# Kernel optimization log

Measured on AMD Instinct MI355X. Metric: run time of the kernel, lower is better.

Reference implementation:

```python
import jax, jax.numpy as jnp
import numpy as np
from jax import lax

B, C, H, T = 128, 64, 32, 256


def _xavier(key, shape):
    fan_out, fan_in = shape[-2], shape[-1]
    s = np.sqrt(6.0 / (fan_in + fan_out)).astype(np.float32)
    return jax.random.uniform(key, shape, jnp.float32, -s, s)


def setup_inputs() -> dict:
    key = jax.random.key(0)
    ks = jax.random.split(key, 12)
    x = jax.random.normal(ks[0], (B, C, T), jnp.float32)
    m = jax.random.uniform(ks[1], (B, C, T), jnp.float32)
    d = jax.random.uniform(ks[2], (B, C, T), jnp.float32)
    Wf = _xavier(ks[3], (C, H, H))
    Vf = _xavier(ks[4], (C, H, 3))
    cf = _xavier(ks[5], (C, H, 1))[:, :, 0]          # (C, H)
    Wb = _xavier(ks[6], (C, H, H))
    Vb = _xavier(ks[7], (C, H, 3))
    cb = _xavier(ks[8], (C, H, 1))[:, :, 0]          # (C, H)
    U = _xavier(ks[9], (C, 1, 2 * H))[:, 0, :]        # (C, 2H)
    c0 = 0.1 * jax.random.normal(ks[10], (C,), jnp.float32)
    return {"x": x, "m": m, "d": d, "Wf": Wf, "Vf": Vf, "cf": cf,
            "Wb": Wb, "Vb": Vb, "cb": cb, "U": U, "c0": c0}


def _mrnn(x, m, d, Wf, Vf, cf, Wb, Vb, cb, U, c0):
    act = jax.nn.relu
    Tn = x.shape[-1]
    pad = lambda a: jnp.pad(a, ((0, 0), (0, 0), (1, 1)), mode="edge")  # replication pad
    feats = jnp.stack([pad(x), pad(m), pad(d)], axis=-1)   # (B, C, T+2, 3)
    # forward RNN sees padded times 0..T-1 (orig t-1); backward sees padded T+1..2 (orig t+1)
    in_f = jnp.transpose(feats[:, :, :Tn], (2, 0, 1, 3))               # (T, B, C, 3)
    in_b = jnp.transpose(feats[:, :, 2:Tn + 2][:, :, ::-1], (2, 0, 1, 3))

    def scan_rnn(W, V, c, inp):
        def step(h, v):
            # per-channel block-diagonal matmul: batched tiny GEMM over C
            hn = act(jnp.einsum("chk,bck->bch", W, h)
                     + jnp.einsum("chj,bcj->bch", V, v) + c)
            return hn, hn
        h0 = jnp.zeros((x.shape[0], W.shape[0], W.shape[1]), x.dtype)
        return lax.scan(step, h0, inp)[1]                  # (T, B, C, H)

    hf = scan_rnn(Wf, Vf, cf, in_f)
    hb = scan_rnn(Wb, Vb, cb, in_b)[::-1]                  # align backward states with t
    hcat = jnp.concatenate([hf, hb], axis=-1)              # (T, B, C, 2H)
    out = act(jnp.einsum("ck,tbck->tbc", U, hcat) + c0)    # (T, B, C)
    return jnp.transpose(out, (1, 2, 0))                   # (B, C, T)


def reference(x, m, d, Wf, Vf, cf, Wb, Vb, cb, U, c0):
    return _mrnn(x, m, d, Wf, Vf, cf, Wb, Vb, cb, U, c0)
```

## Files before the change

kernel.cpp:

```cpp
#include <hip/hip_runtime.h>

constexpr int Bn = 128, Cn = 64, Hn = 32, Tn = 256;

typedef __attribute__((ext_vector_type(8))) short short8;
typedef __attribute__((ext_vector_type(2))) float f32x2;
typedef __attribute__((ext_vector_type(4))) float f32x4;
typedef __attribute__((ext_vector_type(4))) unsigned int u32x4;

__device__ __forceinline__ unsigned pk_hi(unsigned y, unsigned x) {
  return __builtin_amdgcn_perm(y, x, 0x07060302u);
}

__device__ __forceinline__ void wsplit(float w, short& hi, short& lo) {
  unsigned u = __float_as_uint(w);
  float r = w - __uint_as_float(u & 0xffff0000u);
  unsigned ru = __float_as_uint(r) + 0x8000u;
  hi = (short)(u >> 16);
  lo = (short)(ru >> 16);
}

__global__ __launch_bounds__(64, 1)
void mrnn_scan(const float* __restrict__ x, const float* __restrict__ m,
               const float* __restrict__ d,
               const float* __restrict__ Wf, const float* __restrict__ Vf,
               const float* __restrict__ cf,
               const float* __restrict__ Wb, const float* __restrict__ Vb,
               const float* __restrict__ cb,
               const float* __restrict__ U,
               float* __restrict__ pf_out, float* __restrict__ pb_out) {
  const int bid = blockIdx.x;
  const int dir = bid >> 9;
  const int c   = (bid >> 3) & (Cn - 1);
  const int g   = bid & 7;
  const int tid = threadIdx.x;
  const int q = tid >> 4;
  const int n = tid & 15;
  const int b = g * 16 + n;

  const float* W  = dir ? Wb : Wf;
  const float* V  = dir ? Vb : Vf;
  const float* cc = dir ? cb : cf;

  const int ra0 = 8 * (n >> 2) + (n & 3);
  const int ra1 = ra0 + 4;
  short8 A0h, A0l, A1h, A1l;
#pragma unroll
  for (int j = 0; j < 8; ++j) {
    short hi, lo;
    wsplit(W[(c * Hn + ra0) * Hn + 8 * q + j], hi, lo); A0h[j] = hi; A0l[j] = lo;
    wsplit(W[(c * Hn + ra1) * Hn + 8 * q + j], hi, lo); A1h[j] = hi; A1l[j] = lo;
  }

  f32x4 v0xv, v0yv, v0zv, bs0v, uu0v;
  f32x4 v1xv, v1yv, v1zv, bs1v, uu1v;
#pragma unroll
  for (int r = 0; r < 4; ++r) {
    const int row0 = 8 * q + r, row1 = row0 + 4;
    const float* vp0 = V + (c * Hn + row0) * 3;
    v0xv[r] = vp0[0]; v0yv[r] = vp0[1]; v0zv[r] = vp0[2];
    bs0v[r] = cc[c * Hn + row0];
    uu0v[r] = U[c * 2 * Hn + dir * Hn + row0];
    const float* vp1 = V + (c * Hn + row1) * 3;
    v1xv[r] = vp1[0]; v1yv[r] = vp1[1]; v1zv[r] = vp1[2];
    bs1v[r] = cc[c * Hn + row1];
    uu1v[r] = U[c * 2 * Hn + dir * Hn + row1];
  }

  u32x4 Bh = {0u, 0u, 0u, 0u};
  u32x4 Bl = {0u, 0u, 0u, 0u};
  const f32x4 z4 = {0.f, 0.f, 0.f, 0.f};

  const long base = ((long)b * Cn + c) * Tn;
  const float* px = x + base;
  const float* pm = m + base;
  const float* pd = d + base;
  float* pout = (dir ? pb_out : pf_out) + base;

  float cx, cm2, cd2;
  f32x4 qx0, qx1, qm0, qm1, qd0, qd1;
  if (!dir) {
    cx = px[0]; cm2 = pm[0]; cd2 = pd[0];
    qx0 = *(const f32x4*)px;        qx1 = *(const f32x4*)(px + 4);
    qm0 = *(const f32x4*)pm;        qm1 = *(const f32x4*)(pm + 4);
    qd0 = *(const f32x4*)pd;        qd1 = *(const f32x4*)(pd + 4);
  } else {
    cx = px[Tn - 1]; cm2 = pm[Tn - 1]; cd2 = pd[Tn - 1];
    qx0 = *(const f32x4*)(px + Tn - 8); qx1 = *(const f32x4*)(px + Tn - 4);
    qm0 = *(const f32x4*)(pm + Tn - 8); qm1 = *(const f32x4*)(pm + Tn - 4);
    qd0 = *(const f32x4*)(pd + Tn - 8); qd1 = *(const f32x4*)(pd + Tn - 4);
  }

  for (int t0 = 0; t0 < Tn; t0 += 8) {
    int qn_ = dir ? (Tn - 16 - t0) : (t0 + 8);
    if (qn_ < 0) qn_ = 0;
    if (qn_ > Tn - 8) qn_ = Tn - 8;
    const f32x4 nx0 = *(const f32x4*)(px + qn_), nx1 = *(const f32x4*)(px + qn_ + 4);
    const f32x4 nm0 = *(const f32x4*)(pm + qn_), nm1 = *(const f32x4*)(pm + qn_ + 4);
    const f32x4 nd0 = *(const f32x4*)(pd + qn_), nd1 = *(const f32x4*)(pd + qn_ + 4);

    float vxa[8] = {qx0.x, qx0.y, qx0.z, qx0.w, qx1.x, qx1.y, qx1.z, qx1.w};
    float vma[8] = {qm0.x, qm0.y, qm0.z, qm0.w, qm1.x, qm1.y, qm1.z, qm1.w};
    float vda[8] = {qd0.x, qd0.y, qd0.z, qd0.w, qd1.x, qd1.y, qd1.z, qd1.w};
    float inx[8], inm[8], ind[8];
    inx[0] = cx; inm[0] = cm2; ind[0] = cd2;
    if (!dir) {
#pragma unroll
      for (int k = 1; k < 8; ++k) {
        inx[k] = vxa[k - 1]; inm[k] = vma[k - 1]; ind[k] = vda[k - 1];
      }
      cx = vxa[7]; cm2 = vma[7]; cd2 = vda[7];
    } else {
#pragma unroll
      for (int k = 1; k < 8; ++k) {
        inx[k] = vxa[8 - k]; inm[k] = vma[8 - k]; ind[k] = vda[8 - k];
      }
      cx = vxa[0]; cm2 = vma[0]; cd2 = vda[0];
    }

    float pacc[8];
#pragma unroll
    for (int u = 0; u < 8; ++u) {
      const float ix = inx[u], im = inm[u], idv = ind[u];
      const f32x4 ix4 = {ix, ix, ix, ix};
      const f32x4 im4 = {im, im, im, im};
      const f32x4 id4 = {idv, idv, idv, idv};
      f32x4 vi0 = __builtin_elementwise_fma(v0xv, ix4,
                    __builtin_elementwise_fma(v0yv, im4,
                      __builtin_elementwise_fma(v0zv, id4, bs0v)));
      f32x4 vi1 = __builtin_elementwise_fma(v1xv, ix4,
                    __builtin_elementwise_fma(v1yv, im4,
                      __builtin_elementwise_fma(v1zv, id4, bs1v)));
      const short8 bh = __builtin_bit_cast(short8, Bh);
      const short8 bl = __builtin_bit_cast(short8, Bl);
      f32x4 s0 = __builtin_amdgcn_mfma_f32_16x16x32_bf16(A0l, bh, vi0, 0, 0, 0);
      f32x4 s1 = __builtin_amdgcn_mfma_f32_16x16x32_bf16(A1l, bh, vi1, 0, 0, 0);
      f32x4 a0 = __builtin_amdgcn_mfma_f32_16x16x32_bf16(A0h, bh, z4, 0, 0, 0);
      f32x4 a1 = __builtin_amdgcn_mfma_f32_16x16x32_bf16(A1h, bh, z4, 0, 0, 0);
      s0 = __builtin_amdgcn_mfma_f32_16x16x32_bf16(A0h, bl, s0, 0, 0, 0);
      s1 = __builtin_amdgcn_mfma_f32_16x16x32_bf16(A1h, bl, s1, 0, 0, 0);
      f32x4 acc0 = __builtin_elementwise_max(a0 + s0, z4);
      f32x4 acc1 = __builtin_elementwise_max(a1 + s1, z4);
      f32x4 pp = uu0v * acc0;
      pp = __builtin_elementwise_fma(uu1v, acc1, pp);
      const f32x2 ph = __builtin_shufflevector(pp, pp, 0, 1) +
                       __builtin_shufflevector(pp, pp, 2, 3);
      pacc[u] = ph[0] + ph[1];
      const unsigned h00 = __float_as_uint(acc0[0]), h01 = __float_as_uint(acc0[1]);
      const unsigned h02 = __float_as_uint(acc0[2]), h03 = __float_as_uint(acc0[3]);
      const unsigned h10 = __float_as_uint(acc1[0]), h11 = __float_as_uint(acc1[1]);
      const unsigned h12 = __float_as_uint(acc1[2]), h13 = __float_as_uint(acc1[3]);
      Bh[0] = pk_hi(h01, h00); Bh[1] = pk_hi(h03, h02);
      Bh[2] = pk_hi(h11, h10); Bh[3] = pk_hi(h13, h12);
      unsigned ru[8];
#pragma unroll
      for (int r = 0; r < 4; ++r) {
        ru[r]     = __float_as_uint(acc0[r] - __uint_as_float(__float_as_uint(acc0[r]) & 0xffff0000u)) + 0x8000u;
        ru[4 + r] = __float_as_uint(acc1[r] - __uint_as_float(__float_as_uint(acc1[r]) & 0xffff0000u)) + 0x8000u;
      }
      Bl[0] = pk_hi(ru[1], ru[0]); Bl[1] = pk_hi(ru[3], ru[2]);
      Bl[2] = pk_hi(ru[5], ru[4]); Bl[3] = pk_hi(ru[7], ru[6]);
    }
#pragma unroll
    for (int u = 0; u < 8; ++u) pacc[u] += __shfl_xor(pacc[u], 16);
#pragma unroll
    for (int u = 0; u < 8; ++u) pacc[u] += __shfl_xor(pacc[u], 32);

    if (q == 0) {
      if (!dir) {
        f32x4 o0 = {pacc[0], pacc[1], pacc[2], pacc[3]};
        f32x4 o1 = {pacc[4], pacc[5], pacc[6], pacc[7]};
        *(f32x4*)(pout + t0) = o0;
        *(f32x4*)(pout + t0 + 4) = o1;
      } else {
        f32x4 o0 = {pacc[7], pacc[6], pacc[5], pacc[4]};
        f32x4 o1 = {pacc[3], pacc[2], pacc[1], pacc[0]};
        *(f32x4*)(pout + (Tn - 8 - t0)) = o0;
        *(f32x4*)(pout + (Tn - 4 - t0)) = o1;
      }
    }
    qx0 = nx0; qx1 = nx1; qm0 = nm0; qm1 = nm1; qd0 = nd0; qd1 = nd1;
  }
}

__global__ __launch_bounds__(256)
void mrnn_combine(const float* __restrict__ pb, const float* __restrict__ c0,
                  float* __restrict__ out) {
  const int i4 = blockIdx.x * 256 + threadIdx.x;
  const int c = (i4 >> 6) & (Cn - 1);
  const float c0v = c0[c];
  float4 a = ((const float4*)out)[i4];
  const float4 bb = ((const float4*)pb)[i4];
  a.x = fmaxf(a.x + bb.x + c0v, 0.f);
  a.y = fmaxf(a.y + bb.y + c0v, 0.f);
  a.z = fmaxf(a.z + bb.z + c0v, 0.f);
  a.w = fmaxf(a.w + bb.w + c0v, 0.f);
  ((float4*)out)[i4] = a;
}

extern "C" void kernel_launch(void* const* d_in, const int* in_sizes, int n_in,
                              void* d_out, int out_size, void* d_ws, size_t ws_size,
                              hipStream_t stream) {
  const float* x  = (const float*)d_in[0];
  const float* m  = (const float*)d_in[1];
  const float* dd = (const float*)d_in[2];
  const float* Wf = (const float*)d_in[3];
  const float* Vf = (const float*)d_in[4];
  const float* cf = (const float*)d_in[5];
  const float* Wb = (const float*)d_in[6];
  const float* Vb = (const float*)d_in[7];
  const float* cb = (const float*)d_in[8];
  const float* U  = (const float*)d_in[9];
  const float* c0 = (const float*)d_in[10];
  float* out = (float*)d_out;
  float* pb  = (float*)d_ws;

  mrnn_scan<<<1024, 64, 0, stream>>>(x, m, dd, Wf, Vf, cf, Wb, Vb, cb, U, out, pb);
  mrnn_combine<<<(Bn * Cn * Tn) / (256 * 4), 256, 0, stream>>>(pb, c0, out);
}
```

Measured before the change: 153.9 us.

## Interleave two independent batch chains per wave to hide recurrence latency

Each wave now runs two independent 16-batch recurrence chains, interleaved step by step, and the grid is halved from 1024 to 512 blocks. The goal is to fill the latency of the serial MFMA → relu → repack chain with independent work from the other chain, instead of depending on occupancy of single-chain waves. This raises register pressure and halves the number of waves. With launch_bounds(64,1) and 256 CUs, fewer waves per CU could leave some SIMDs idle.

Result: slower. 202.7 us (+31.7%).

```diff
diff --git a/kernel.cpp b/kernel.cpp
--- a/kernel.cpp
+++ b/kernel.cpp
@@ -29,13 +29,12 @@
                const float* __restrict__ U,
                float* __restrict__ pf_out, float* __restrict__ pb_out) {
   const int bid = blockIdx.x;
-  const int dir = bid >> 9;
-  const int c   = (bid >> 3) & (Cn - 1);
-  const int g   = bid & 7;
+  const int dir = bid >> 8;
+  const int c   = (bid >> 2) & (Cn - 1);
+  const int gp  = bid & 3;
   const int tid = threadIdx.x;
   const int q = tid >> 4;
   const int n = tid & 15;
-  const int b = g * 16 + n;
 
   const float* W  = dir ? Wb : Wf;
   const float* V  = dir ? Vb : Vf;
@@ -66,119 +65,147 @@
     uu1v[r] = U[c * 2 * Hn + dir * Hn + row1];
   }
 
-  u32x4 Bh = {0u, 0u, 0u, 0u};
-  u32x4 Bl = {0u, 0u, 0u, 0u};
   const f32x4 z4 = {0.f, 0.f, 0.f, 0.f};
 
-  const long base = ((long)b * Cn + c) * Tn;
-  const float* px = x + base;
-  const float* pm = m + base;
-  const float* pd = d + base;
-  float* pout = (dir ? pb_out : pf_out) + base;
-
-  float cx, cm2, cd2;
-  f32x4 qx0, qx1, qm0, qm1, qd0, qd1;
-  if (!dir) {
-    cx = px[0]; cm2 = pm[0]; cd2 = pd[0];
-    qx0 = *(const f32x4*)px;        qx1 = *(const f32x4*)(px + 4);
-    qm0 = *(const f32x4*)pm;        qm1 = *(const f32x4*)(pm + 4);
-    qd0 = *(const f32x4*)pd;        qd1 = *(const f32x4*)(pd + 4);
-  } else {
-    cx = px[Tn - 1]; cm2 = pm[Tn - 1]; cd2 = pd[Tn - 1];
-    qx0 = *(const f32x4*)(px + Tn - 8); qx1 = *(const f32x4*)(px + Tn - 4);
-    qm0 = *(const f32x4*)(pm + Tn - 8); qm1 = *(const f32x4*)(pm + Tn - 4);
-    qd0 = *(const f32x4*)(pd + Tn - 8); qd1 = *(const f32x4*)(pd + Tn - 4);
+  u32x4 BhA[2], BlA[2];
+  const float *pxA[2], *pmA[2], *pdA[2];
+  float* poutA[2];
+  float cxA[2], cmA[2], cdA[2];
+  f32x4 qx0A[2], qx1A[2], qm0A[2], qm1A[2], qd0A[2], qd1A[2];
+#pragma unroll
+  for (int ch = 0; ch < 2; ++ch) {
+    BhA[ch] = u32x4{0u, 0u, 0u, 0u};
+    BlA[ch] = u32x4{0u, 0u, 0u, 0u};
+    const int b = (gp * 2 + ch) * 16 + n;
+    const long base = ((long)b * Cn + c) * Tn;
+    pxA[ch] = x + base;
+    pmA[ch] = m + base;
+    pdA[ch] = d + base;
+    poutA[ch] = (dir ? pb_out : pf_out) + base;
+    if (!dir) {
+      cxA[ch] = pxA[ch][0]; cmA[ch] = pmA[ch][0]; cdA[ch] = pdA[ch][0];
+      qx0A[ch] = *(const f32x4*)pxA[ch];        qx1A[ch] = *(const f32x4*)(pxA[ch] + 4);
+      qm0A[ch] = *(const f32x4*)pmA[ch];        qm1A[ch] = *(const f32x4*)(pmA[ch] + 4);
+      qd0A[ch] = *(const f32x4*)pdA[ch];        qd1A[ch] = *(const f32x4*)(pdA[ch] + 4);
+    } else {
+      cxA[ch] = pxA[ch][Tn - 1]; cmA[ch] = pmA[ch][Tn - 1]; cdA[ch] = pdA[ch][Tn - 1];
+      qx0A[ch] = *(const f32x4*)(pxA[ch] + Tn - 8); qx1A[ch] = *(const f32x4*)(pxA[ch] + Tn - 4);
+      qm0A[ch] = *(const f32x4*)(pmA[ch] + Tn - 8); qm1A[ch] = *(const f32x4*)(pmA[ch] + Tn - 4);
+      qd0A[ch] = *(const f32x4*)(pdA[ch] + Tn - 8); qd1A[ch] = *(const f32x4*)(pdA[ch] + Tn - 4);
+    }
   }
 
   for (int t0 = 0; t0 < Tn; t0 += 8) {
     int qn_ = dir ? (Tn - 16 - t0) : (t0 + 8);
     if (qn_ < 0) qn_ = 0;
     if (qn_ > Tn - 8) qn_ = Tn - 8;
-    const f32x4 nx0 = *(const f32x4*)(px + qn_), nx1 = *(const f32x4*)(px + qn_ + 4);
-    const f32x4 nm0 = *(const f32x4*)(pm + qn_), nm1 = *(const f32x4*)(pm + qn_ + 4);
-    const f32x4 nd0 = *(const f32x4*)(pd + qn_), nd1 = *(const f32x4*)(pd + qn_ + 4);
-
-    float vxa[8] = {qx0.x, qx0.y, qx0.z, qx0.w, qx1.x, qx1.y, qx1.z, qx1.w};
-    float vma[8] = {qm0.x, qm0.y, qm0.z, qm0.w, qm1.x, qm1.y, qm1.z, qm1.w};
-    float vda[8] = {qd0.x, qd0.y, qd0.z, qd0.w, qd1.x, qd1.y, qd1.z, qd1.w};
-    float inx[8], inm[8], ind[8];
-    inx[0] = cx; inm[0] = cm2; ind[0] = cd2;
-    if (!dir) {
-#pragma unroll
-      for (int k = 1; k < 8; ++k) {
-        inx[k] = vxa[k - 1]; inm[k] = vma[k - 1]; ind[k] = vda[k - 1];
+
+    f32x4 nx0[2], nx1[2], nm0[2], nm1[2], nd0[2], nd1[2];
+    float inx[2][8], inm[2][8], ind[2][8];
+#pragma unroll
+    for (int ch = 0; ch < 2; ++ch) {
+      nx0[ch] = *(const f32x4*)(pxA[ch] + qn_); nx1[ch] = *(const f32x4*)(pxA[ch] + qn_ + 4);
+      nm0[ch] = *(const f32x4*)(pmA[ch] + qn_); nm1[ch] = *(const f32x4*)(pmA[ch] + qn_ + 4);
+      nd0[ch] = *(const f32x4*)(pdA[ch] + qn_); nd1[ch] = *(const f32x4*)(pdA[ch] + qn_ + 4);
+
+      float vxa[8] = {qx0A[ch].x, qx0A[ch].y, qx0A[ch].z, qx0A[ch].w,
+                      qx1A[ch].x, qx1A[ch].y, qx1A[ch].z, qx1A[ch].w};
+      float vma[8] = {qm0A[ch].x, qm0A[ch].y, qm0A[ch].z, qm0A[ch].w,
+                      qm1A[ch].x, qm1A[ch].y, qm1A[ch].z, qm1A[ch].w};
+      float vda[8] = {qd0A[ch].x, qd0A[ch].y, qd0A[ch].z, qd0A[ch].w,
+                      qd1A[ch].x, qd1A[ch].y, qd1A[ch].z, qd1A[ch].w};
+      inx[ch][0] = cxA[ch]; inm[ch][0] = cmA[ch]; ind[ch][0] = cdA[ch];
+      if (!dir) {
+#pragma unroll
+        for (int k = 1; k < 8; ++k) {
+          inx[ch][k] = vxa[k - 1]; inm[ch][k] = vma[k - 1]; ind[ch][k] = vda[k - 1];
+        }
+        cxA[ch] = vxa[7]; cmA[ch] = vma[7]; cdA[ch] = vda[7];
+      } else {
+#pragma unroll
+        for (int k = 1; k < 8; ++k) {
+          inx[ch][k] = vxa[8 - k]; inm[ch][k] = vma[8 - k]; ind[ch][k] = vda[8 - k];
+        }
+        cxA[ch] = vxa[0]; cmA[ch] = vma[0]; cdA[ch] = vda[0];
       }
-      cx = vxa[7]; cm2 = vma[7]; cd2 = vda[7];
-    } else {
-#pragma unroll
-      for (int k = 1; k < 8; ++k) {
-        inx[k] = vxa[8 - k]; inm[k] = vma[8 - k]; ind[k] = vda[8 - k];
+    }
+
+    float pacc[2][8];
+#pragma unroll
+    for (int u = 0; u < 8; ++u) {
+#pragma unroll
+      for (int ch = 0; ch < 2; ++ch) {
+        const float ix = inx[ch][u], im = inm[ch][u], idv = ind[ch][u];
+        const f32x4 ix4 = {ix, ix, ix, ix};
+        const f32x4 im4 = {im, im, im, im};
+        const f32x4 id4 = {idv, idv, idv, idv};
+        f32x4 vi0 = __builtin_elementwise_fma(v0xv, ix4,
+                      __builtin_elementwise_fma(v0yv, im4,
+                        __builtin_elementwise_fma(v0zv, id4, bs0v)));
+        f32x4 vi1 = __builtin_elementwise_fma(v1xv, ix4,
+                      __builtin_elementwise_fma(v1yv, im4,
+                        __builtin_elementwise_fma(v1zv, id4, bs1v)));
+        const short8 bh = __builtin_bit_cast(short8, BhA[ch]);
+        const short8 bl = __builtin_bit_cast(short8, BlA[ch]);
+        f32x4 s0 = __builtin_amdgcn_mfma_f32_16x16x32_bf16(A0l, bh, vi0, 0, 0, 0);
+        f32x4 s1 = __builtin_amdgcn_mfma_f32_16x16x32_bf16(A1l, bh, vi1, 0, 0, 0);
+        f32x4 a0 = __builtin_amdgcn_mfma_f32_16x16x32_bf16(A0h, bh, z4, 0, 0, 0);
+        f32x4 a1 = __builtin_amdgcn_mfma_f32_16x16x32_bf16(A1h, bh, z4, 0, 0, 0);
+        s0 = __builtin_amdgcn_mfma_f32_16x16x32_bf16(A0h, bl, s0, 0, 0, 0);
+        s1 = __builtin_amdgcn_mfma_f32_16x16x32_bf16(A1h, bl, s1, 0, 0, 0);
+        f32x4 acc0 = __builtin_elementwise_max(a0 + s0, z4);
+        f32x4 acc1 = __builtin_elementwise_max(a1 + s1, z4);
+        f32x4 pp = uu0v * acc0;
+        pp = __builtin_elementwise_fma(uu1v, acc1, pp);
+        const f32x2 ph = __builtin_shufflevector(pp, pp, 0, 1) +
+                         __builtin_shufflevector(pp, pp, 2, 3);
+        pacc[ch][u] = ph[0] + ph[1];
+        const unsigned h00 = __float_as_uint(acc0[0]), h01 = __float_as_uint(acc0[1]);
+        const unsigned h02 = __float_as_uint(acc0[2]), h03 = __float_as_uint(acc0[3]);
+        const unsigned h10 = __float_as_uint(acc1[0]), h11 = __float_as_uint(acc1[1]);
+        const unsigned h12 = __float_as_uint(acc1[2]), h13 = __float_as_uint(acc1[3]);
+        BhA[ch][0] = pk_hi(h01, h00); BhA[ch][1] = pk_hi(h03, h02);
+        BhA[ch][2] = pk_hi(h11, h10); BhA[ch][3] = pk_hi(h13, h12);
+        unsigned ru[8];
+#pragma unroll
+        for (int r = 0; r < 4; ++r) {
+          ru[r]     = __float_as_uint(acc0[r] - __uint_as_float(__float_as_uint(acc0[r]) & 0xffff0000u)) + 0x8000u;
+          ru[4 + r] = __float_as_uint(acc1[r] - __uint_as_float(__float_as_uint(acc1[r]) & 0xffff0000u)) + 0x8000u;
+        }
+        BlA[ch][0] = pk_hi(ru[1], ru[0]); BlA[ch][1] = pk_hi(ru[3], ru[2]);
+        BlA[ch][2] = pk_hi(ru[5], ru[4]); BlA[ch][3] = pk_hi(ru[7], ru[6]);
       }
-      cx = vxa[0]; cm2 = vma[0]; cd2 = vda[0];
-    }
-
-    float pacc[8];
-#pragma unroll
-    for (int u = 0; u < 8; ++u) {
-      const float ix = inx[u], im = inm[u], idv = ind[u];
-      const f32x4 ix4 = {ix, ix, ix, ix};
-      const f32x4 im4 = {im, im, im, im};
-      const f32x4 id4 = {idv, idv, idv, idv};
-      f32x4 vi0 = __builtin_elementwise_fma(v0xv, ix4,
-                    __builtin_elementwise_fma(v0yv, im4,
-                      __builtin_elementwise_fma(v0zv, id4, bs0v)));
-      f32x4 vi1 = __builtin_elementwise_fma(v1xv, ix4,
-                    __builtin_elementwise_fma(v1yv, im4,
-                      __builtin_elementwise_fma(v1zv, id4, bs1v)));
-      const short8 bh = __builtin_bit_cast(short8, Bh);
-      const short8 bl = __builtin_bit_cast(short8, Bl);
-      f32x4 s0 = __builtin_amdgcn_mfma_f32_16x16x32_bf16(A0l, bh, vi0, 0, 0, 0);
-      f32x4 s1 = __builtin_amdgcn_mfma_f32_16x16x32_bf16(A1l, bh, vi1, 0, 0, 0);
-      f32x4 a0 = __builtin_amdgcn_mfma_f32_16x16x32_bf16(A0h, bh, z4, 0, 0, 0);
-      f32x4 a1 = __builtin_amdgcn_mfma_f32_16x16x32_bf16(A1h, bh, z4, 0, 0, 0);
-      s0 = __builtin_amdgcn_mfma_f32_16x16x32_bf16(A0h, bl, s0, 0, 0, 0);
-      s1 = __builtin_amdgcn_mfma_f32_16x16x32_bf16(A1h, bl, s1, 0, 0, 0);
-      f32x4 acc0 = __builtin_elementwise_max(a0 + s0, z4);
-      f32x4 acc1 = __builtin_elementwise_max(a1 + s1, z4);
-      f32x4 pp = uu0v * acc0;
-      pp = __builtin_elementwise_fma(uu1v, acc1, pp);
-      const f32x2 ph = __builtin_shufflevector(pp, pp, 0, 1) +
-                       __builtin_shufflevector(pp, pp, 2, 3);
-      pacc[u] = ph[0] + ph[1];
-      const unsigned h00 = __float_as_uint(acc0[0]), h01 = __float_as_uint(acc0[1]);
-      const unsigned h02 = __float_as_uint(acc0[2]), h03 = __float_as_uint(acc0[3]);
-      const unsigned h10 = __float_as_uint(acc1[0]), h11 = __float_as_uint(acc1[1]);
-      const unsigned h12 = __float_as_uint(acc1[2]), h13 = __float_as_uint(acc1[3]);
-      Bh[0] = pk_hi(h01, h00); Bh[1] = pk_hi(h03, h02);
-      Bh[2] = pk_hi(h11, h10); Bh[3] = pk_hi(h13, h12);
-      unsigned ru[8];
-#pragma unroll
-      for (int r = 0; r < 4; ++r) {
-        ru[r]     = __float_as_uint(acc0[r] - __uint_as_float(__float_as_uint(acc0[r]) & 0xffff0000u)) + 0x8000u;
-        ru[4 + r] = __float_as_uint(acc1[r] - __uint_as_float(__float_as_uint(acc1[r]) & 0xffff0000u)) + 0x8000u;
+    }
+#pragma unroll
+    for (int ch = 0; ch < 2; ++ch) {
+#pragma unroll
+      for (int u = 0; u < 8; ++u) pacc[ch][u] += __shfl_xor(pacc[ch][u], 16);
+#pragma unroll
+      for (int u = 0; u < 8; ++u) pacc[ch][u] += __shfl_xor(pacc[ch][u], 32);
+    }
+
+    if (q == 0) {
+#pragma unroll
+      for (int ch = 0; ch < 2; ++ch) {
+        if (!dir) {
+          f32x4 o0 = {pacc[ch][0], pacc[ch][1], pacc[ch][2], pacc[ch][3]};
+          f32x4 o1 = {pacc[ch][4], pacc[ch][5], pacc[ch][6], pacc[ch][7]};
+          *(f32x4*)(poutA[ch] + t0) = o0;
+          *(f32x4*)(poutA[ch] + t0 + 4) = o1;
+        } else {
+          f32x4 o0 = {pacc[ch][7], pacc[ch][6], pacc[ch][5], pacc[ch][4]};
+          f32x4 o1 = {pacc[ch][3], pacc[ch][2], pacc[ch][1], pacc[ch][0]};
+          *(f32x4*)(poutA[ch] + (Tn - 8 - t0)) = o0;
+          *(f32x4*)(poutA[ch] + (Tn - 4 - t0)) = o1;
+        }
       }
-      Bl[0] = pk_hi(ru[1], ru[0]); Bl[1] = pk_hi(ru[3], ru[2]);
-      Bl[2] = pk_hi(ru[5], ru[4]); Bl[3] = pk_hi(ru[7], ru[6]);
-    }
-#pragma unroll
-    for (int u = 0; u < 8; ++u) pacc[u] += __shfl_xor(pacc[u], 16);
-#pragma unroll
-    for (int u = 0; u < 8; ++u) pacc[u] += __shfl_xor(pacc[u], 32);
-
-    if (q == 0) {
-      if (!dir) {
-        f32x4 o0 = {pacc[0], pacc[1], pacc[2], pacc[3]};
-        f32x4 o1 = {pacc[4], pacc[5], pacc[6], pacc[7]};
-        *(f32x4*)(pout + t0) = o0;
-        *(f32x4*)(pout + t0 + 4) = o1;
-      } else {
-        f32x4 o0 = {pacc[7], pacc[6], pacc[5], pacc[4]};
-        f32x4 o1 = {pacc[3], pacc[2], pacc[1], pacc[0]};
-        *(f32x4*)(pout + (Tn - 8 - t0)) = o0;
-        *(f32x4*)(pout + (Tn - 4 - t0)) = o1;
-      }
-    }
-    qx0 = nx0; qx1 = nx1; qm0 = nm0; qm1 = nm1; qd0 = nd0; qd1 = nd1;
+    }
+#pragma unroll
+    for (int ch = 0; ch < 2; ++ch) {
+      qx0A[ch] = nx0[ch]; qx1A[ch] = nx1[ch];
+      qm0A[ch] = nm0[ch]; qm1A[ch] = nm1[ch];
+      qd0A[ch] = nd0[ch]; qd1A[ch] = nd1[ch];
+    }
   }
 }
 
@@ -214,6 +241,6 @@
   float* out = (float*)d_out;
   float* pb  = (float*)d_ws;
 
-  mrnn_scan<<<1024, 64, 0, stream>>>(x, m, dd, Wf, Vf, cf, Wb, Vb, cb, U, out, pb);
+  mrnn_scan<<<512, 64, 0, stream>>>(x, m, dd, Wf, Vf, cf, Wb, Vb, cb, U, out, pb);
   mrnn_combine<<<(Bn * Cn * Tn) / (256 * 4), 256, 0, stream>>>(pb, c0, out);
 }
```
